# Kernel optimization log

Hardware: AMD Instinct MI355X
Metric: run time of the kernel (lower is better)

Reference implementation:

```python
import jax, jax.numpy as jnp
import numpy as np

D, H, HD, L, P, DF = 256, 8, 32, 4, 4, 1024
BS, NQ = 8, 900
SHAPES = np.array([[128, 128], [64, 64], [32, 32], [16, 16]], dtype=np.int64)
NV = int((SHAPES[:, 0] * SHAPES[:, 1]).sum())  # 21760


def setup_inputs():
    ks = jax.random.split(jax.random.key(0), 16)
    p = lambda i, s: jax.random.normal(ks[i], s, jnp.float32) * 0.02
    lsi = np.concatenate([[0], np.cumsum(SHAPES[:, 0] * SHAPES[:, 1])[:-1]]).astype(np.int64)
    return dict(
        tgt=jax.random.normal(ks[0], (BS, NQ, D), jnp.float32),
        query_pos=jax.random.normal(ks[1], (BS, NQ, D), jnp.float32),
        reference_points=jax.random.uniform(ks[2], (BS, NQ, L, 2), jnp.float32),
        src=jax.random.normal(ks[3], (BS, NV, D), jnp.float32),
        sa_in_w=p(4, (3 * D, D)), sa_in_b=jnp.zeros((3 * D,), jnp.float32),
        sa_out_w=p(5, (D, D)), sa_out_b=jnp.zeros((D,), jnp.float32),
        ln2_g=jnp.ones((D,), jnp.float32), ln2_b=jnp.zeros((D,), jnp.float32),
        off_w=p(6, (H * L * P * 2, D)),
        off_b=jax.random.uniform(ks[7], (H * L * P * 2,), jnp.float32, -2.0, 2.0),
        aw_w=p(8, (H * L * P, D)), aw_b=jnp.zeros((H * L * P,), jnp.float32),
        val_w=p(9, (D, D)), val_b=jnp.zeros((D,), jnp.float32),
        out_w=p(10, (D, D)), out_b=jnp.zeros((D,), jnp.float32),
        ln1_g=jnp.ones((D,), jnp.float32), ln1_b=jnp.zeros((D,), jnp.float32),
        ffn1_w=p(11, (DF, D)), ffn1_b=jnp.zeros((DF,), jnp.float32),
        ffn2_w=p(12, (D, DF)), ffn2_b=jnp.zeros((D,), jnp.float32),
        ln3_g=jnp.ones((D,), jnp.float32), ln3_b=jnp.zeros((D,), jnp.float32),
        spatial_shapes=SHAPES,
        level_start_index=lsi,
    )


def _ln(x, g, b):
    m = x.mean(-1, keepdims=True)
    v = ((x - m) ** 2).mean(-1, keepdims=True)
    return (x - m) * jax.lax.rsqrt(v + 1e-5) * g + b


def _msda_core(query, value, ref, off_w, off_b, aw_w, aw_b, spatial_shapes):
    # query: (bs,nq,D); value: (bs,NV,H,HD); ref: (bs,nq,L,2) normalized in [0,1]
    bs, nq, _ = query.shape
    off = (query @ off_w.T + off_b).reshape(bs, nq, H, L, P, 2)
    aw = jax.nn.softmax((query @ aw_w.T + aw_b).reshape(bs, nq, H, L * P), axis=-1)
    aw = aw.reshape(bs, nq, H, L, P)
    # offset normalizer is (W, H) per level
    norm = jnp.asarray(np.ascontiguousarray(spatial_shapes[:, ::-1]), jnp.float32)
    loc = ref[:, :, None, :, None, :] + off / norm[None, None, None, :, None, :]
    starts = np.concatenate([[0], np.cumsum(spatial_shapes[:, 0] * spatial_shapes[:, 1])])
    out = jnp.zeros((bs, nq, H, HD), query.dtype)
    for l in range(L):
        hh, ww = int(spatial_shapes[l, 0]), int(spatial_shapes[l, 1])
        v = value[:, int(starts[l]):int(starts[l + 1])].transpose(0, 2, 1, 3)  # (bs,H,hw,HD)
        lx = loc[:, :, :, l, :, 0] * ww - 0.5  # (bs,nq,H,P), align_corners=False
        ly = loc[:, :, :, l, :, 1] * hh - 0.5
        x0, y0 = jnp.floor(lx), jnp.floor(ly)
        tx, ty = lx - x0, ly - y0
        samp = jnp.zeros((bs, H, nq, P, HD), query.dtype)
        for dy, wy in ((0, 1.0 - ty), (1, ty)):
            for dx, wx in ((0, 1.0 - tx), (1, tx)):
                xi, yi = x0 + dx, y0 + dy
                valid = (xi >= 0) & (xi < ww) & (yi >= 0) & (yi < hh)  # zero padding
                idx = (jnp.clip(yi, 0, hh - 1) * ww + jnp.clip(xi, 0, ww - 1)).astype(jnp.int32)
                idxg = idx.transpose(0, 2, 1, 3).reshape(bs, H, nq * P, 1)  # (bs,H,nq*P,1)
                g = jnp.take_along_axis(v, idxg, axis=2).reshape(bs, H, nq, P, HD)
                w = (wy * wx * valid.astype(query.dtype)).transpose(0, 2, 1, 3)[..., None]
                samp = samp + g * w
        out = out + jnp.einsum('bhqpd,bqhp->bqhd', samp, aw[:, :, :, l, :])
    return out.reshape(bs, nq, H * HD)


def _forward(tgt, query_pos, reference_points, src,
             sa_in_w, sa_in_b, sa_out_w, sa_out_b, ln2_g, ln2_b,
             off_w, off_b, aw_w, aw_b, val_w, val_b, out_w, out_b, ln1_g, ln1_b,
             ffn1_w, ffn1_b, ffn2_w, ffn2_b, ln3_g, ln3_b,
             spatial_shapes):
    bs, nq, _ = tgt.shape
    # --- self attention (q=k=tgt+pos, v=tgt) ---
    qk = tgt + query_pos
    wq, wk, wv = sa_in_w[:D], sa_in_w[D:2 * D], sa_in_w[2 * D:]
    bq, bk, bv = sa_in_b[:D], sa_in_b[D:2 * D], sa_in_b[2 * D:]
    q = (qk @ wq.T + bq).reshape(bs, nq, H, HD)
    k = (qk @ wk.T + bk).reshape(bs, nq, H, HD)
    v = (tgt @ wv.T + bv).reshape(bs, nq, H, HD)
    attn = jax.nn.softmax(jnp.einsum('bqhd,bkhd->bhqk', q, k) / np.sqrt(HD).astype(np.float32), axis=-1)
    sa = jnp.einsum('bhqk,bkhd->bqhd', attn, v).reshape(bs, nq, D) @ sa_out_w.T + sa_out_b
    tgt = _ln(tgt + sa, ln2_g, ln2_b)
    # --- multi-scale deformable cross attention (mmcv: residual inside) ---
    value = (src @ val_w.T + val_b).reshape(bs, -1, H, HD)
    ca = _msda_core(tgt + query_pos, value, reference_points, off_w, off_b, aw_w, aw_b, spatial_shapes)
    ca = ca @ out_w.T + out_b + tgt  # mmcv MSDA adds identity internally
    tgt = _ln(tgt + ca, ln1_g, ln1_b)
    # --- FFN ---
    ffn = jax.nn.relu(tgt @ ffn1_w.T + ffn1_b) @ ffn2_w.T + ffn2_b
    return _ln(tgt + ffn, ln3_g, ln3_b)


def reference(tgt, query_pos, reference_points, src,
              sa_in_w, sa_in_b, sa_out_w, sa_out_b, ln2_g, ln2_b,
              off_w, off_b, aw_w, aw_b, val_w, val_b, out_w, out_b, ln1_g, ln1_b,
              ffn1_w, ffn1_b, ffn2_w, ffn2_b, ln3_g, ln3_b,
              spatial_shapes, level_start_index):
    del level_start_index  # level splits recomputed statically from spatial_shapes
    return _forward(tgt, query_pos, reference_points, src,
                    sa_in_w, sa_in_b, sa_out_w, sa_out_b, ln2_g, ln2_b,
                    off_w, off_b, aw_w, aw_b, val_w, val_b, out_w, out_b, ln1_g, ln1_b,
                    ffn1_w, ffn1_b, ffn2_w, ffn2_b, ln3_g, ln3_b,
                    spatial_shapes)
```

## Files before the change

kernel.cpp:

```cpp
#include <hip/hip_runtime.h>
#include <math.h>

#define D_   256
#define H_   8
#define HD_  32
#define L_   4
#define P_   4
#define DF_  1024
#define BS_  8
#define NQ_  900
#define NV_  21760
#define M1   (BS_*NQ_)
#define MV   (BS_*NV_)
#define QKVW 768
#define OAW  384
#define KS_  8
#define KCH  113

typedef __attribute__((ext_vector_type(8))) short short8v;
typedef __attribute__((ext_vector_type(4))) float float4v;
typedef unsigned short ushort_t;
typedef unsigned int uint_t;

__device__ __forceinline__ ushort_t f2bf(float f) {
    uint_t u = __float_as_uint(f);
    u += 0x7FFFu + ((u >> 16) & 1u);
    return (ushort_t)(u >> 16);
}
__device__ __forceinline__ float bf2f(ushort_t h) {
    return __uint_as_float(((uint_t)h) << 16);
}

template<bool ADD2, bool RELU, bool ADDRES>
__global__ __launch_bounds__(256) void gemm_mfma(const float* __restrict__ A,
                                                 const float* __restrict__ A2,
                                                 const float* __restrict__ Wt,
                                                 const float* __restrict__ bias,
                                                 const float* __restrict__ res,
                                                 float* __restrict__ C,
                                                 int M, int K, int ldc, int coffs)
{
    __shared__ short Al[8 * 64 * 8];
    __shared__ short Wl[8 * 4 * 64 * 8];

    const int tid = threadIdx.x;
    const int bm = blockIdx.y * 128, bn = blockIdx.x * 64;

    const int l = tid & 63, w = tid >> 6;
    const int mbase = (w & 1) * 4, nbase = (w >> 1) * 2;
    float4v acc[4][2];
    #pragma unroll
    for (int m = 0; m < 4; m++)
        #pragma unroll
        for (int n = 0; n < 2; n++)
            acc[m][n] = (float4v){0.f, 0.f, 0.f, 0.f};

    const int arow  = tid >> 1;
    const int arow_c = min(bm + arow, M - 1);
    const int khalf = (tid & 1) * 16;
    const float* ap  = A + (size_t)arow_c * K + khalf;
    const float* ap2 = ADD2 ? (A2 + (size_t)arow_c * K + khalf) : nullptr;

    const int wrow = tid >> 2;
    const int kq   = (tid & 3) * 64;

    for (int ks = 0; ks < K; ks += 256) {
        __syncthreads();
        {
            const float* wp = Wt + (size_t)(bn + wrow) * K + ks + kq;
            #pragma unroll
            for (int grp = 0; grp < 8; grp++) {
                float4 f0 = *(const float4*)(wp + grp * 8);
                float4 f1 = *(const float4*)(wp + grp * 8 + 4);
                short8v v;
                v[0] = (short)f2bf(f0.x); v[1] = (short)f2bf(f0.y);
                v[2] = (short)f2bf(f0.z); v[3] = (short)f2bf(f0.w);
                v[4] = (short)f2bf(f1.x); v[5] = (short)f2bf(f1.y);
                v[6] = (short)f2bf(f1.z); v[7] = (short)f2bf(f1.w);
                int kg = (tid & 3) * 8 + grp;
                int kc = kg >> 2, kin = kg & 3;
                int off = (((kc * 4 + (wrow >> 4)) * 64) + kin * 16 + (wrow & 15)) * 8;
                *(short8v*)&Wl[off] = v;
            }
        }
        float4 r0, r1, r2, r3;
        {
            const float* p = ap + ks;
            r0 = *(const float4*)(p + 0);  r1 = *(const float4*)(p + 4);
            r2 = *(const float4*)(p + 8);  r3 = *(const float4*)(p + 12);
            if (ADD2) {
                const float* p2 = ap2 + ks;
                float4 s0 = *(const float4*)(p2 + 0), s1 = *(const float4*)(p2 + 4);
                float4 s2 = *(const float4*)(p2 + 8), s3 = *(const float4*)(p2 + 12);
                r0.x += s0.x; r0.y += s0.y; r0.z += s0.z; r0.w += s0.w;
                r1.x += s1.x; r1.y += s1.y; r1.z += s1.z; r1.w += s1.w;
                r2.x += s2.x; r2.y += s2.y; r2.z += s2.z; r2.w += s2.w;
                r3.x += s3.x; r3.y += s3.y; r3.z += s3.z; r3.w += s3.w;
            }
        }

        for (int kc = 0; kc < 8; kc++) {
            {
                short8v v0, v1;
                v0[0] = (short)f2bf(r0.x); v0[1] = (short)f2bf(r0.y);
                v0[2] = (short)f2bf(r0.z); v0[3] = (short)f2bf(r0.w);
                v0[4] = (short)f2bf(r1.x); v0[5] = (short)f2bf(r1.y);
                v0[6] = (short)f2bf(r1.z); v0[7] = (short)f2bf(r1.w);
                v1[0] = (short)f2bf(r2.x); v1[1] = (short)f2bf(r2.y);
                v1[2] = (short)f2bf(r2.z); v1[3] = (short)f2bf(r2.w);
                v1[4] = (short)f2bf(r3.x); v1[5] = (short)f2bf(r3.y);
                v1[6] = (short)f2bf(r3.z); v1[7] = (short)f2bf(r3.w);
                int kg = (tid & 1) * 2;
                int off0 = (((arow >> 4) * 64) + kg * 16 + (arow & 15)) * 8;
                int off1 = (((arow >> 4) * 64) + (kg + 1) * 16 + (arow & 15)) * 8;
                *(short8v*)&Al[off0] = v0;
                *(short8v*)&Al[off1] = v1;
            }
            if (kc < 7) {
                const float* p = ap + ks + (kc + 1) * 32;
                r0 = *(const float4*)(p + 0);  r1 = *(const float4*)(p + 4);
                r2 = *(const float4*)(p + 8);  r3 = *(const float4*)(p + 12);
                if (ADD2) {
                    const float* p2 = ap2 + ks + (kc + 1) * 32;
                    float4 s0 = *(const float4*)(p2 + 0), s1 = *(const float4*)(p2 + 4);
                    float4 s2 = *(const float4*)(p2 + 8), s3 = *(const float4*)(p2 + 12);
                    r0.x += s0.x; r0.y += s0.y; r0.z += s0.z; r0.w += s0.w;
                    r1.x += s1.x; r1.y += s1.y; r1.z += s1.z; r1.w += s1.w;
                    r2.x += s2.x; r2.y += s2.y; r2.z += s2.z; r2.w += s2.w;
                    r3.x += s3.x; r3.y += s3.y; r3.z += s3.z; r3.w += s3.w;
                }
            }
            __syncthreads();

            short8v af0 = *(const short8v*)&Al[((mbase + 0) * 64 + l) * 8];
            short8v af1 = *(const short8v*)&Al[((mbase + 1) * 64 + l) * 8];
            short8v af2 = *(const short8v*)&Al[((mbase + 2) * 64 + l) * 8];
            short8v af3 = *(const short8v*)&Al[((mbase + 3) * 64 + l) * 8];
            short8v bf0 = *(const short8v*)&Wl[((kc * 4 + nbase + 0) * 64 + l) * 8];
            short8v bf1 = *(const short8v*)&Wl[((kc * 4 + nbase + 1) * 64 + l) * 8];

            acc[0][0] = __builtin_amdgcn_mfma_f32_16x16x32_bf16(af0, bf0, acc[0][0], 0, 0, 0);
            acc[0][1] = __builtin_amdgcn_mfma_f32_16x16x32_bf16(af0, bf1, acc[0][1], 0, 0, 0);
            acc[1][0] = __builtin_amdgcn_mfma_f32_16x16x32_bf16(af1, bf0, acc[1][0], 0, 0, 0);
            acc[1][1] = __builtin_amdgcn_mfma_f32_16x16x32_bf16(af1, bf1, acc[1][1], 0, 0, 0);
            acc[2][0] = __builtin_amdgcn_mfma_f32_16x16x32_bf16(af2, bf0, acc[2][0], 0, 0, 0);
            acc[2][1] = __builtin_amdgcn_mfma_f32_16x16x32_bf16(af2, bf1, acc[2][1], 0, 0, 0);
            acc[3][0] = __builtin_amdgcn_mfma_f32_16x16x32_bf16(af3, bf0, acc[3][0], 0, 0, 0);
            acc[3][1] = __builtin_amdgcn_mfma_f32_16x16x32_bf16(af3, bf1, acc[3][1], 0, 0, 0);

            __syncthreads();
        }
    }

    #pragma unroll
    for (int n = 0; n < 2; n++) {
        int gc = bn + nbase * 16 + n * 16 + (l & 15);
        float bc = bias[gc];
        #pragma unroll
        for (int m = 0; m < 4; m++) {
            int gr0 = bm + mbase * 16 + m * 16 + (l >> 4) * 4;
            #pragma unroll
            for (int r = 0; r < 4; r++) {
                int gr = gr0 + r;
                if (gr >= M) continue;
                float v = acc[m][n][r] + bc;
                if (ADDRES) v += res[(size_t)gr * ldc + coffs + gc];
                if (RELU)   v = fmaxf(v, 0.f);
                C[(size_t)gr * ldc + coffs + gc] = v;
            }
        }
    }
}

__global__ __launch_bounds__(256) void gemm_val_bf16(const float* __restrict__ A,
                                                     const float* __restrict__ Wt,
                                                     const float* __restrict__ bias,
                                                     ushort_t* __restrict__ C)
{
    __shared__ short Al[8 * 64 * 8];
    __shared__ short Wl[8 * 4 * 64 * 8];

    const int tid = threadIdx.x;
    const int bm = blockIdx.y * 128, bn = blockIdx.x * 64;

    {
        const int wrow = tid >> 2;
        const int kq   = (tid & 3) * 64;
        const float* wp = Wt + (size_t)(bn + wrow) * D_ + kq;
        #pragma unroll
        for (int grp = 0; grp < 8; grp++) {
            float4 f0 = *(const float4*)(wp + grp * 8);
            float4 f1 = *(const float4*)(wp + grp * 8 + 4);
            short8v v;
            v[0] = (short)f2bf(f0.x); v[1] = (short)f2bf(f0.y);
            v[2] = (short)f2bf(f0.z); v[3] = (short)f2bf(f0.w);
            v[4] = (short)f2bf(f1.x); v[5] = (short)f2bf(f1.y);
            v[6] = (short)f2bf(f1.z); v[7] = (short)f2bf(f1.w);
            int kg = (tid & 3) * 8 + grp;
            int kc = kg >> 2, kin = kg & 3;
            int off = (((kc * 4 + (wrow >> 4)) * 64) + kin * 16 + (wrow & 15)) * 8;
            *(short8v*)&Wl[off] = v;
        }
    }

    const int arow = tid >> 1;
    const int khalf = (tid & 1) * 16;
    const float* ap = A + (size_t)(bm + arow) * D_ + khalf;

    float4 r0, r1, r2, r3;
    r0 = *(const float4*)(ap + 0);  r1 = *(const float4*)(ap + 4);
    r2 = *(const float4*)(ap + 8);  r3 = *(const float4*)(ap + 12);

    const int l = tid & 63, w = tid >> 6;
    const int mbase = (w & 1) * 4, nbase = (w >> 1) * 2;
    float4v acc[4][2];
    #pragma unroll
    for (int m = 0; m < 4; m++)
        #pragma unroll
        for (int n = 0; n < 2; n++)
            acc[m][n] = (float4v){0.f, 0.f, 0.f, 0.f};

    __syncthreads();

    for (int kc = 0; kc < 8; kc++) {
        {
            short8v v0, v1;
            v0[0] = (short)f2bf(r0.x); v0[1] = (short)f2bf(r0.y);
            v0[2] = (short)f2bf(r0.z); v0[3] = (short)f2bf(r0.w);
            v0[4] = (short)f2bf(r1.x); v0[5] = (short)f2bf(r1.y);
            v0[6] = (short)f2bf(r1.z); v0[7] = (short)f2bf(r1.w);
            v1[0] = (short)f2bf(r2.x); v1[1] = (short)f2bf(r2.y);
            v1[2] = (short)f2bf(r2.z); v1[3] = (short)f2bf(r2.w);
            v1[4] = (short)f2bf(r3.x); v1[5] = (short)f2bf(r3.y);
            v1[6] = (short)f2bf(r3.z); v1[7] = (short)f2bf(r3.w);
            int kg = (tid & 1) * 2;
            int off0 = (((arow >> 4) * 64) + kg * 16 + (arow & 15)) * 8;
            int off1 = (((arow >> 4) * 64) + (kg + 1) * 16 + (arow & 15)) * 8;
            *(short8v*)&Al[off0] = v0;
            *(short8v*)&Al[off1] = v1;
        }
        if (kc < 7) {
            const float* np = ap + (kc + 1) * 32;
            r0 = *(const float4*)(np + 0);  r1 = *(const float4*)(np + 4);
            r2 = *(const float4*)(np + 8);  r3 = *(const float4*)(np + 12);
        }
        __syncthreads();

        short8v af0 = *(const short8v*)&Al[((mbase + 0) * 64 + l) * 8];
        short8v af1 = *(const short8v*)&Al[((mbase + 1) * 64 + l) * 8];
        short8v af2 = *(const short8v*)&Al[((mbase + 2) * 64 + l) * 8];
        short8v af3 = *(const short8v*)&Al[((mbase + 3) * 64 + l) * 8];
        short8v bf0 = *(const short8v*)&Wl[((kc * 4 + nbase + 0) * 64 + l) * 8];
        short8v bf1 = *(const short8v*)&Wl[((kc * 4 + nbase + 1) * 64 + l) * 8];

        acc[0][0] = __builtin_amdgcn_mfma_f32_16x16x32_bf16(af0, bf0, acc[0][0], 0, 0, 0);
        acc[0][1] = __builtin_amdgcn_mfma_f32_16x16x32_bf16(af0, bf1, acc[0][1], 0, 0, 0);
        acc[1][0] = __builtin_amdgcn_mfma_f32_16x16x32_bf16(af1, bf0, acc[1][0], 0, 0, 0);
        acc[1][1] = __builtin_amdgcn_mfma_f32_16x16x32_bf16(af1, bf1, acc[1][1], 0, 0, 0);
        acc[2][0] = __builtin_amdgcn_mfma_f32_16x16x32_bf16(af2, bf0, acc[2][0], 0, 0, 0);
        acc[2][1] = __builtin_amdgcn_mfma_f32_16x16x32_bf16(af2, bf1, acc[2][1], 0, 0, 0);
        acc[3][0] = __builtin_amdgcn_mfma_f32_16x16x32_bf16(af3, bf0, acc[3][0], 0, 0, 0);
        acc[3][1] = __builtin_amdgcn_mfma_f32_16x16x32_bf16(af3, bf1, acc[3][1], 0, 0, 0);

        __syncthreads();
    }

    #pragma unroll
    for (int n = 0; n < 2; n++) {
        int gc = bn + nbase * 16 + n * 16 + (l & 15);
        float bc = bias[gc];
        #pragma unroll
        for (int m = 0; m < 4; m++) {
            int gr = bm + mbase * 16 + m * 16 + (l >> 4) * 4;
            #pragma unroll
            for (int r = 0; r < 4; r++)
                C[(size_t)(gr + r) * D_ + gc] = f2bf(acc[m][n][r] + bc);
        }
    }
}

#define ATK 64
__global__ __launch_bounds__(128) void attn_kernel(const float* __restrict__ QKV,
                                                   float* __restrict__ pml,
                                                   float* __restrict__ pacc)
{
    const int b = blockIdx.z, h = blockIdx.y;
    const int qb = blockIdx.x & 7, ks = blockIdx.x >> 3;
    const int q0 = qb * 128;
    const int kstart = ks * KCH;
    const int kend   = min(NQ_, kstart + KCH);
    const int tid  = threadIdx.x;
    const int wave = tid >> 6, lane = tid & 63;
    const int qi = lane & 31, half = lane >> 5;

    __shared__ float Ksm[ATK][HD_];
    __shared__ float Vsm[ATK][HD_];

    const int q_a = q0 + wave * 64 + qi * 2;
    const int q_b = q_a + 1;
    const int qa_c = min(q_a, NQ_ - 1);
    const int qb_c = min(q_b, NQ_ - 1);

    const float scale = 0.17677669529663687f;
    float Qa[16], Qb[16];
    {
        const float* pa = QKV + ((size_t)(b * NQ_ + qa_c)) * QKVW + h * HD_ + half * 16;
        const float* pb = QKV + ((size_t)(b * NQ_ + qb_c)) * QKVW + h * HD_ + half * 16;
        #pragma unroll
        for (int i = 0; i < 16; i += 4) {
            float4 va = *(const float4*)&pa[i];
            float4 vb = *(const float4*)&pb[i];
            Qa[i] = va.x * scale; Qa[i+1] = va.y * scale; Qa[i+2] = va.z * scale; Qa[i+3] = va.w * scale;
            Qb[i] = vb.x * scale; Qb[i+1] = vb.y * scale; Qb[i+2] = vb.z * scale; Qb[i+3] = vb.w * scale;
        }
    }

    float ma = -INFINITY, la = 0.f, mb = -INFINITY, lb = 0.f;
    float aa[16], ab[16];
    #pragma unroll
    for (int i = 0; i < 16; i++) { aa[i] = 0.f; ab[i] = 0.f; }

    for (int j0 = kstart; j0 < kend; j0 += ATK) {
        const int jn = min(ATK, kend - j0);
        __syncthreads();
        for (int f = tid; f < ATK * HD_ / 4; f += 128) {
            int j = f >> 3, d4 = (f & 7) << 2;
            if (j < jn) {
                const float* kp = QKV + ((size_t)(b * NQ_ + j0 + j)) * QKVW + 256 + h * HD_ + d4;
                *(float4*)&Ksm[j][d4] = *(const float4*)kp;
                *(float4*)&Vsm[j][d4] = *(const float4*)(kp + 256);
            }
        }
        __syncthreads();

        for (int j = 0; j < jn; j++) {
            float kr[16];
            #pragma unroll
            for (int i = 0; i < 16; i += 4) {
                float4 kv = *(const float4*)&Ksm[j][half * 16 + i];
                kr[i] = kv.x; kr[i+1] = kv.y; kr[i+2] = kv.z; kr[i+3] = kv.w;
            }
            float sa0 = 0.f, sa1 = 0.f, sa2 = 0.f, sa3 = 0.f;
            float sb0 = 0.f, sb1 = 0.f, sb2 = 0.f, sb3 = 0.f;
            #pragma unroll
            for (int i = 0; i < 16; i += 4) {
                sa0 += Qa[i] * kr[i];     sa1 += Qa[i+1] * kr[i+1];
                sa2 += Qa[i+2] * kr[i+2]; sa3 += Qa[i+3] * kr[i+3];
                sb0 += Qb[i] * kr[i];     sb1 += Qb[i+1] * kr[i+1];
                sb2 += Qb[i+2] * kr[i+2]; sb3 += Qb[i+3] * kr[i+3];
            }
            float sA = (sa0 + sa1) + (sa2 + sa3);
            float sB = (sb0 + sb1) + (sb2 + sb3);
            sA += __shfl_xor(sA, 32);
            sB += __shfl_xor(sB, 32);

            float vr[16];
            #pragma unroll
            for (int i = 0; i < 16; i += 4) {
                float4 vv = *(const float4*)&Vsm[j][half * 16 + i];
                vr[i] = vv.x; vr[i+1] = vv.y; vr[i+2] = vv.z; vr[i+3] = vv.w;
            }

            if (sA > ma) {
                float sc = __expf(ma - sA);
                la *= sc;
                #pragma unroll
                for (int i = 0; i < 16; i++) aa[i] *= sc;
                ma = sA;
            }
            float pA = __expf(sA - ma);
            la += pA;
            #pragma unroll
            for (int i = 0; i < 16; i++) aa[i] += pA * vr[i];

            if (sB > mb) {
                float sc = __expf(mb - sB);
                lb *= sc;
                #pragma unroll
                for (int i = 0; i < 16; i++) ab[i] *= sc;
                mb = sB;
            }
            float pB = __expf(sB - mb);
            lb += pB;
            #pragma unroll
            for (int i = 0; i < 16; i++) ab[i] += pB * vr[i];
        }
    }

    const int bh = b * H_ + h;
    if (q_a < NQ_) {
        size_t base = (((size_t)bh * KS_ + ks) * NQ_ + q_a) * 32 + half * 16;
        #pragma unroll
        for (int i = 0; i < 16; i += 4) {
            float4 v = make_float4(aa[i], aa[i+1], aa[i+2], aa[i+3]);
            *(float4*)&pacc[base + i] = v;
        }
        if (half == 0) {
            size_t mb_ = (((size_t)bh * KS_ + ks) * NQ_ + q_a) * 2;
            pml[mb_] = ma; pml[mb_ + 1] = la;
        }
    }
    if (q_b < NQ_) {
        size_t base = (((size_t)bh * KS_ + ks) * NQ_ + q_b) * 32 + half * 16;
        #pragma unroll
        for (int i = 0; i < 16; i += 4) {
            float4 v = make_float4(ab[i], ab[i+1], ab[i+2], ab[i+3]);
            *(float4*)&pacc[base + i] = v;
        }
        if (half == 0) {
            size_t mb_ = (((size_t)bh * KS_ + ks) * NQ_ + q_b) * 2;
            pml[mb_] = mb; pml[mb_ + 1] = lb;
        }
    }
}

__global__ __launch_bounds__(256) void attn_combine(const float* __restrict__ pml,
                                                    const float* __restrict__ pacc,
                                                    float* __restrict__ SA)
{
    const int g  = threadIdx.x >> 5;
    const int ch = threadIdx.x & 31;
    const int t  = blockIdx.x * 8 + g;
    const int bh = t / NQ_, q = t - bh * NQ_;

    float mv[KS_], lv[KS_];
    float M = -INFINITY;
    #pragma unroll
    for (int i = 0; i < KS_; i++) {
        size_t mb = (((size_t)bh * KS_ + i) * NQ_ + q) * 2;
        mv[i] = pml[mb]; lv[i] = pml[mb + 1];
        M = fmaxf(M, mv[i]);
    }
    float L = 0.f, acc = 0.f;
    #pragma unroll
    for (int i = 0; i < KS_; i++) {
        float wgt = __expf(mv[i] - M);
        L += lv[i] * wgt;
        acc += wgt * pacc[(((size_t)bh * KS_ + i) * NQ_ + q) * 32 + ch];
    }
    const int b = bh >> 3, h = bh & 7;
    SA[((size_t)(b * NQ_ + q)) * D_ + h * HD_ + ch] = acc / L;
}

__global__ __launch_bounds__(64) void ln_kernel(const float* __restrict__ X,
                                                const float* __restrict__ Y,
                                                const float* __restrict__ g,
                                                const float* __restrict__ bt,
                                                float* __restrict__ out)
{
    const int row = blockIdx.x;
    const int lane = threadIdx.x;
    const size_t base = (size_t)row * D_ + lane * 4;
    float4 x = *(const float4*)&X[base];
    float4 y = *(const float4*)&Y[base];
    float v0 = x.x + y.x, v1 = x.y + y.y, v2 = x.z + y.z, v3 = x.w + y.w;
    float s = v0 + v1 + v2 + v3;
    #pragma unroll
    for (int o = 32; o; o >>= 1) s += __shfl_xor(s, o);
    float mean = s * (1.f / D_);
    float d0 = v0 - mean, d1 = v1 - mean, d2 = v2 - mean, d3 = v3 - mean;
    float ss = d0 * d0 + d1 * d1 + d2 * d2 + d3 * d3;
    #pragma unroll
    for (int o = 32; o; o >>= 1) ss += __shfl_xor(ss, o);
    float rstd = rsqrtf(ss * (1.f / D_) + 1e-5f);
    float4 gg = *(const float4*)&g[lane * 4];
    float4 bb = *(const float4*)&bt[lane * 4];
    float4 o4 = make_float4(d0 * rstd * gg.x + bb.x, d1 * rstd * gg.y + bb.y,
                            d2 * rstd * gg.z + bb.z, d3 * rstd * gg.w + bb.w);
    *(float4*)&out[base] = o4;
}

__global__ __launch_bounds__(256) void aw_softmax_kernel(float* __restrict__ offaw)
{
    int t = blockIdx.x * 256 + threadIdx.x;
    if (t >= M1 * H_) return;
    const int bq = t >> 3, h = t & 7;
    float* p = offaw + (size_t)bq * OAW + 256 + h * 16;
    float v[16];
    #pragma unroll
    for (int i = 0; i < 16; i += 4) {
        float4 q = *(const float4*)&p[i];
        v[i] = q.x; v[i+1] = q.y; v[i+2] = q.z; v[i+3] = q.w;
    }
    float m = v[0];
    #pragma unroll
    for (int i = 1; i < 16; i++) m = fmaxf(m, v[i]);
    float s = 0.f;
    #pragma unroll
    for (int i = 0; i < 16; i++) { v[i] = __expf(v[i] - m); s += v[i]; }
    float inv = 1.f / s;
    #pragma unroll
    for (int i = 0; i < 16; i += 4) {
        float4 q = make_float4(v[i] * inv, v[i+1] * inv, v[i+2] * inv, v[i+3] * inv);
        *(float4*)&p[i] = q;
    }
}

__global__ __launch_bounds__(256) void msda_kernel(const ushort_t* __restrict__ value,
                                                   const float* __restrict__ offaw,
                                                   const float* __restrict__ ref,
                                                   float* __restrict__ out)
{
    const int g    = threadIdx.x >> 5;
    const int lane = threadIdx.x & 31;
    const int t    = blockIdx.x * 8 + g;
    const int h  = t & 7;
    const int bq = t >> 3;
    const int b  = bq / NQ_;
    const float* offp = offaw + (size_t)bq * OAW + h * (L_ * P_ * 2);
    const float* awp  = offaw + (size_t)bq * OAW + 256 + h * (L_ * P_);
    const float* refp = ref + (size_t)bq * (L_ * 2);
    const ushort_t* vb = value + ((size_t)b * NV_) * D_ + h * HD_ + lane;

    float acc = 0.f;
    const int LW[4] = {128, 64, 32, 16};
    const int LS[4] = {0, 16384, 20480, 21504};

    #pragma unroll
    for (int l = 0; l < L_; l++) {
        const int wi = LW[l];
        const float Wf = (float)wi;
        float rx = refp[2 * l], ry = refp[2 * l + 1];
        #pragma unroll
        for (int p = 0; p < P_; p++) {
            float ox = offp[(l * P_ + p) * 2];
            float oy = offp[(l * P_ + p) * 2 + 1];
            float a  = awp[l * P_ + p];
            float lx = rx * Wf + ox - 0.5f;
            float ly = ry * Wf + oy - 0.5f;
            float x0f = floorf(lx), y0f = floorf(ly);
            float fx = lx - x0f, fy = ly - y0f;
            int x0 = (int)x0f, y0 = (int)y0f;
            #pragma unroll
            for (int dy = 0; dy < 2; dy++) {
                int yi = y0 + dy;
                if (yi < 0 || yi >= wi) continue;
                float wy = dy ? fy : 1.f - fy;
                #pragma unroll
                for (int dx = 0; dx < 2; dx++) {
                    int xi = x0 + dx;
                    if (xi < 0 || xi >= wi) continue;
                    float w = wy * (dx ? fx : 1.f - fx) * a;
                    acc += w * bf2f(vb[(size_t)(LS[l] + yi * wi + xi) * D_]);
                }
            }
        }
    }
    out[(size_t)bq * D_ + h * HD_ + lane] = acc;
}

extern "C" void kernel_launch(void* const* d_in, const int* in_sizes, int n_in,
                              void* d_out, int out_size, void* d_ws, size_t ws_size,
                              hipStream_t stream)
{
    const float* tgt      = (const float*)d_in[0];
    const float* qpos     = (const float*)d_in[1];
    const float* ref      = (const float*)d_in[2];
    const float* src      = (const float*)d_in[3];
    const float* sa_in_w  = (const float*)d_in[4];
    const float* sa_in_b  = (const float*)d_in[5];
    const float* sa_out_w = (const float*)d_in[6];
    const float* sa_out_b = (const float*)d_in[7];
    const float* ln2_g    = (const float*)d_in[8];
    const float* ln2_b    = (const float*)d_in[9];
    const float* off_w    = (const float*)d_in[10];
    const float* off_b    = (const float*)d_in[11];
    const float* aw_w     = (const float*)d_in[12];
    const float* aw_b     = (const float*)d_in[13];
    const float* val_w    = (const float*)d_in[14];
    const float* val_b    = (const float*)d_in[15];
    const float* out_w    = (const float*)d_in[16];
    const float* out_b    = (const float*)d_in[17];
    const float* ln1_g    = (const float*)d_in[18];
    const float* ln1_b    = (const float*)d_in[19];
    const float* ffn1_w   = (const float*)d_in[20];
    const float* ffn1_b   = (const float*)d_in[21];
    const float* ffn2_w   = (const float*)d_in[22];
    const float* ffn2_b   = (const float*)d_in[23];
    const float* ln3_g    = (const float*)d_in[24];
    const float* ln3_b    = (const float*)d_in[25];

    float* ws      = (float*)d_ws;
    ushort_t* value = (ushort_t*)ws;
    float* qkv   = ws + 22282240;
    float* battn = qkv + (size_t)M1 * QKVW;
    float* b2    = battn + (size_t)M1 * D_;
    float* b4    = b2 + (size_t)M1 * D_;
    float* pml   = b4 + (size_t)M1 * D_;
    float* pacc  = pml + (size_t)M1 * H_ * KS_ * 2;
    float* bsa   = qkv;
    float* offaw = qkv + (size_t)M1 * D_;
    float* bmsda = qkv;
    float* bca   = battn;
    float* hid   = pml;
    float* bffn  = qkv;
    float* out   = (float*)d_out;

    const dim3 g57_4(4, 57), g57_8(8, 57), g57_2(2, 57), g57_16(16, 57);

    gemm_mfma<true,  false, false><<<g57_8, 256, 0, stream>>>(
        tgt, qpos, sa_in_w, sa_in_b, nullptr, qkv, M1, D_, QKVW, 0);
    gemm_mfma<false, false, false><<<g57_4, 256, 0, stream>>>(
        tgt, nullptr, sa_in_w + 2 * D_ * D_, sa_in_b + 2 * D_, nullptr, qkv, M1, D_, QKVW, 512);
    gemm_val_bf16<<<dim3(D_ / 64, MV / 128), 256, 0, stream>>>(
        src, val_w, val_b, value);
    attn_kernel<<<dim3(8 * KS_, H_, BS_), 128, 0, stream>>>(qkv, pml, pacc);
    attn_combine<<<M1 * H_ / 8, 256, 0, stream>>>(pml, pacc, battn);
    gemm_mfma<false, false, false><<<g57_4, 256, 0, stream>>>(
        battn, nullptr, sa_out_w, sa_out_b, nullptr, bsa, M1, D_, D_, 0);
    ln_kernel<<<M1, 64, 0, stream>>>(tgt, bsa, ln2_g, ln2_b, b2);
    gemm_mfma<true, false, false><<<g57_4, 256, 0, stream>>>(
        b2, qpos, off_w, off_b, nullptr, offaw, M1, D_, OAW, 0);
    gemm_mfma<true, false, false><<<g57_2, 256, 0, stream>>>(
        b2, qpos, aw_w, aw_b, nullptr, offaw, M1, D_, OAW, 256);
    aw_softmax_kernel<<<(M1 * H_ + 255) / 256, 256, 0, stream>>>(offaw);
    msda_kernel<<<M1 * H_ / 8, 256, 0, stream>>>(value, offaw, ref, bmsda);
    gemm_mfma<false, false, true><<<g57_4, 256, 0, stream>>>(
        bmsda, nullptr, out_w, out_b, b2, bca, M1, D_, D_, 0);
    ln_kernel<<<M1, 64, 0, stream>>>(b2, bca, ln1_g, ln1_b, b4);
    gemm_mfma<false, true,  false><<<g57_16, 256, 0, stream>>>(
        b4, nullptr, ffn1_w, ffn1_b, nullptr, hid, M1, D_, DF_, 0);
    gemm_mfma<false, false, false><<<g57_4, 256, 0, stream>>>(
        hid, nullptr, ffn2_w, ffn2_b, nullptr, bffn, M1, DF_, D_, 0);
    ln_kernel<<<M1, 64, 0, stream>>>(b4, bffn, ln3_g, ln3_b, out);
}
```

Before: 868.9 us.

## Replace split-K scalar self-attention with single-pass bf16 MFMA flash attention

Replaces the scalar FP32 self-attention kernel, which split keys into 8 chunks and then needed a separate combine kernel, with one flash-attention kernel. It computes QK^T and PV using bf16 16x16x32 MFMA instructions with an online softmax over 64-key tiles. This removes the partial-result buffers and the combine launch and moves the dot products onto matrix cores. In exchange Q, K, V and P are rounded to bf16, which lowers precision. Grid parallelism also drops to 15x64 blocks, each walking all keys sequentially.

```diff
diff --git a/kernel.cpp b/kernel.cpp
--- a/kernel.cpp
+++ b/kernel.cpp
@@ -14,8 +14,7 @@
 #define MV   (BS_*NV_)
 #define QKVW 768
 #define OAW  384
-#define KS_  8
-#define KCH  113
+#define KT_  64
 
 typedef __attribute__((ext_vector_type(8))) short short8v;
 typedef __attribute__((ext_vector_type(4))) float float4v;
@@ -279,167 +278,146 @@
     }
 }
 
-#define ATK 64
-__global__ __launch_bounds__(128) void attn_kernel(const float* __restrict__ QKV,
-                                                   float* __restrict__ pml,
-                                                   float* __restrict__ pacc)
+__global__ __launch_bounds__(256) void attn_mfma(const float* __restrict__ QKV,
+                                                 float* __restrict__ SA)
 {
-    const int b = blockIdx.z, h = blockIdx.y;
-    const int qb = blockIdx.x & 7, ks = blockIdx.x >> 3;
-    const int q0 = qb * 128;
-    const int kstart = ks * KCH;
-    const int kend   = min(NQ_, kstart + KCH);
-    const int tid  = threadIdx.x;
-    const int wave = tid >> 6, lane = tid & 63;
-    const int qi = lane & 31, half = lane >> 5;
-
-    __shared__ float Ksm[ATK][HD_];
-    __shared__ float Vsm[ATK][HD_];
-
-    const int q_a = q0 + wave * 64 + qi * 2;
-    const int q_b = q_a + 1;
-    const int qa_c = min(q_a, NQ_ - 1);
-    const int qb_c = min(q_b, NQ_ - 1);
+    const int bh = blockIdx.y;
+    const int b = bh >> 3, h = bh & 7;
+    const int q0 = blockIdx.x * 64;
+    const int tid = threadIdx.x, l = tid & 63, w = tid >> 6;
+
+    __shared__ short Ql[4][64][8];
+    __shared__ short Kl[4][64][8];
+    __shared__ short Vl[2][2][64][8];
+    __shared__ short Pl[4][2][64][8];
+    __shared__ float cs[4][16];
 
     const float scale = 0.17677669529663687f;
-    float Qa[16], Qb[16];
+
     {
-        const float* pa = QKV + ((size_t)(b * NQ_ + qa_c)) * QKVW + h * HD_ + half * 16;
-        const float* pb = QKV + ((size_t)(b * NQ_ + qb_c)) * QKVW + h * HD_ + half * 16;
-        #pragma unroll
-        for (int i = 0; i < 16; i += 4) {
-            float4 va = *(const float4*)&pa[i];
-            float4 vb = *(const float4*)&pb[i];
-            Qa[i] = va.x * scale; Qa[i+1] = va.y * scale; Qa[i+2] = va.z * scale; Qa[i+3] = va.w * scale;
-            Qb[i] = vb.x * scale; Qb[i+1] = vb.y * scale; Qb[i+2] = vb.z * scale; Qb[i+3] = vb.w * scale;
-        }
-    }
-
-    float ma = -INFINITY, la = 0.f, mb = -INFINITY, lb = 0.f;
-    float aa[16], ab[16];
-    #pragma unroll
-    for (int i = 0; i < 16; i++) { aa[i] = 0.f; ab[i] = 0.f; }
-
-    for (int j0 = kstart; j0 < kend; j0 += ATK) {
-        const int jn = min(ATK, kend - j0);
+        const int qrow = tid >> 2, dgrp = tid & 3;
+        const int qg = min(q0 + qrow, NQ_ - 1);
+        const float* qp = QKV + ((size_t)(b * NQ_ + qg)) * QKVW + h * HD_ + dgrp * 8;
+        float4 f0 = *(const float4*)qp, f1 = *(const float4*)(qp + 4);
+        short8v v;
+        v[0] = (short)f2bf(f0.x * scale); v[1] = (short)f2bf(f0.y * scale);
+        v[2] = (short)f2bf(f0.z * scale); v[3] = (short)f2bf(f0.w * scale);
+        v[4] = (short)f2bf(f1.x * scale); v[5] = (short)f2bf(f1.y * scale);
+        v[6] = (short)f2bf(f1.z * scale); v[7] = (short)f2bf(f1.w * scale);
+        *(short8v*)&Ql[qrow >> 4][(qrow & 15) + 16 * dgrp][0] = v;
+    }
+    __syncthreads();
+    const short8v qf = *(const short8v*)&Ql[w][l][0];
+
+    float m = -INFINITY, lsum = 0.f;
+    float4v o0 = (float4v){0.f, 0.f, 0.f, 0.f};
+    float4v o1 = (float4v){0.f, 0.f, 0.f, 0.f};
+
+    for (int kt0 = 0; kt0 < NQ_; kt0 += KT_) {
+        {
+            const int krow = tid >> 2, dgrp = tid & 3;
+            const int key = kt0 + krow;
+            float4 f0 = make_float4(0.f,0.f,0.f,0.f), f1 = f0;
+            float4 g0 = f0, g1 = f0;
+            if (key < NQ_) {
+                const float* kp = QKV + ((size_t)(b * NQ_ + key)) * QKVW + 256 + h * HD_ + dgrp * 8;
+                f0 = *(const float4*)kp;       f1 = *(const float4*)(kp + 4);
+                g0 = *(const float4*)(kp+256); g1 = *(const float4*)(kp + 260);
+            }
+            short8v v;
+            v[0] = (short)f2bf(f0.x); v[1] = (short)f2bf(f0.y);
+            v[2] = (short)f2bf(f0.z); v[3] = (short)f2bf(f0.w);
+            v[4] = (short)f2bf(f1.x); v[5] = (short)f2bf(f1.y);
+            v[6] = (short)f2bf(f1.z); v[7] = (short)f2bf(f1.w);
+            *(short8v*)&Kl[krow >> 4][(krow & 15) + 16 * dgrp][0] = v;
+
+            const int kf = krow >> 5;
+            const int lb = 16 * ((krow & 31) >> 3);
+            const int j  = krow & 7;
+            const int d0 = dgrp * 8;
+            Vl[kf][(d0+0)>>4][((d0+0)&15)+lb][j] = (short)f2bf(g0.x);
+            Vl[kf][(d0+1)>>4][((d0+1)&15)+lb][j] = (short)f2bf(g0.y);
+            Vl[kf][(d0+2)>>4][((d0+2)&15)+lb][j] = (short)f2bf(g0.z);
+            Vl[kf][(d0+3)>>4][((d0+3)&15)+lb][j] = (short)f2bf(g0.w);
+            Vl[kf][(d0+4)>>4][((d0+4)&15)+lb][j] = (short)f2bf(g1.x);
+            Vl[kf][(d0+5)>>4][((d0+5)&15)+lb][j] = (short)f2bf(g1.y);
+            Vl[kf][(d0+6)>>4][((d0+6)&15)+lb][j] = (short)f2bf(g1.z);
+            Vl[kf][(d0+7)>>4][((d0+7)&15)+lb][j] = (short)f2bf(g1.w);
+        }
         __syncthreads();
-        for (int f = tid; f < ATK * HD_ / 4; f += 128) {
-            int j = f >> 3, d4 = (f & 7) << 2;
-            if (j < jn) {
-                const float* kp = QKV + ((size_t)(b * NQ_ + j0 + j)) * QKVW + 256 + h * HD_ + d4;
-                *(float4*)&Ksm[j][d4] = *(const float4*)kp;
-                *(float4*)&Vsm[j][d4] = *(const float4*)(kp + 256);
-            }
+
+        float4v s[4];
+        #pragma unroll
+        for (int f = 0; f < 4; f++) {
+            short8v kfr = *(const short8v*)&Kl[f][l][0];
+            s[f] = __builtin_amdgcn_mfma_f32_16x16x32_bf16(
+                kfr, qf, (float4v){0.f, 0.f, 0.f, 0.f}, 0, 0, 0);
+        }
+        if (kt0 + KT_ > NQ_) {
+            #pragma unroll
+            for (int f = 0; f < 4; f++)
+                #pragma unroll
+                for (int r = 0; r < 4; r++)
+                    if (kt0 + f * 16 + (l >> 4) * 4 + r >= NQ_) s[f][r] = -1e30f;
+        }
+
+        float tm = -1e30f;
+        #pragma unroll
+        for (int f = 0; f < 4; f++)
+            #pragma unroll
+            for (int r = 0; r < 4; r++) tm = fmaxf(tm, s[f][r]);
+        tm = fmaxf(tm, __shfl_xor(tm, 16));
+        tm = fmaxf(tm, __shfl_xor(tm, 32));
+        float mnew = fmaxf(m, tm);
+        float c = __expf(m - mnew);
+        m = mnew;
+        float ps = 0.f;
+        #pragma unroll
+        for (int f = 0; f < 4; f++)
+            #pragma unroll
+            for (int r = 0; r < 4; r++) {
+                float p = __expf(s[f][r] - m);
+                s[f][r] = p; ps += p;
+            }
+        ps += __shfl_xor(ps, 16);
+        ps += __shfl_xor(ps, 32);
+        lsum = lsum * c + ps;
+        if ((l >> 4) == 0) cs[w][l & 15] = c;
+        float4 c4 = *(const float4*)&cs[w][(l >> 4) * 4];
+        o0[0] *= c4.x; o0[1] *= c4.y; o0[2] *= c4.z; o0[3] *= c4.w;
+        o1[0] *= c4.x; o1[1] *= c4.y; o1[2] *= c4.z; o1[3] *= c4.w;
+
+        #pragma unroll
+        for (int f = 0; f < 4; f++) {
+            uint_t lo = (uint_t)f2bf(s[f][0]) | ((uint_t)f2bf(s[f][1]) << 16);
+            uint_t hi = (uint_t)f2bf(s[f][2]) | ((uint_t)f2bf(s[f][3]) << 16);
+            int lp = (l & 15) + 16 * ((f & 1) * 2 + ((l >> 4) >> 1));
+            int j0 = ((l >> 4) & 1) * 4;
+            *(uint2*)&Pl[w][f >> 1][lp][j0] = make_uint2(lo, hi);
+        }
+        #pragma unroll
+        for (int kf = 0; kf < 2; kf++) {
+            short8v pa = *(const short8v*)&Pl[w][kf][l][0];
+            short8v v0 = *(const short8v*)&Vl[kf][0][l][0];
+            short8v v1 = *(const short8v*)&Vl[kf][1][l][0];
+            o0 = __builtin_amdgcn_mfma_f32_16x16x32_bf16(pa, v0, o0, 0, 0, 0);
+            o1 = __builtin_amdgcn_mfma_f32_16x16x32_bf16(pa, v1, o1, 0, 0, 0);
         }
         __syncthreads();
-
-        for (int j = 0; j < jn; j++) {
-            float kr[16];
-            #pragma unroll
-            for (int i = 0; i < 16; i += 4) {
-                float4 kv = *(const float4*)&Ksm[j][half * 16 + i];
-                kr[i] = kv.x; kr[i+1] = kv.y; kr[i+2] = kv.z; kr[i+3] = kv.w;
-            }
-            float sa0 = 0.f, sa1 = 0.f, sa2 = 0.f, sa3 = 0.f;
-            float sb0 = 0.f, sb1 = 0.f, sb2 = 0.f, sb3 = 0.f;
-            #pragma unroll
-            for (int i = 0; i < 16; i += 4) {
-                sa0 += Qa[i] * kr[i];     sa1 += Qa[i+1] * kr[i+1];
-                sa2 += Qa[i+2] * kr[i+2]; sa3 += Qa[i+3] * kr[i+3];
-                sb0 += Qb[i] * kr[i];     sb1 += Qb[i+1] * kr[i+1];
-                sb2 += Qb[i+2] * kr[i+2]; sb3 += Qb[i+3] * kr[i+3];
-            }
-            float sA = (sa0 + sa1) + (sa2 + sa3);
-            float sB = (sb0 + sb1) + (sb2 + sb3);
-            sA += __shfl_xor(sA, 32);
-            sB += __shfl_xor(sB, 32);
-
-            float vr[16];
-            #pragma unroll
-            for (int i = 0; i < 16; i += 4) {
-                float4 vv = *(const float4*)&Vsm[j][half * 16 + i];
-                vr[i] = vv.x; vr[i+1] = vv.y; vr[i+2] = vv.z; vr[i+3] = vv.w;
-            }
-
-            if (sA > ma) {
-                float sc = __expf(ma - sA);
-                la *= sc;
-                #pragma unroll
-                for (int i = 0; i < 16; i++) aa[i] *= sc;
-                ma = sA;
-            }
-            float pA = __expf(sA - ma);
-            la += pA;
-            #pragma unroll
-            for (int i = 0; i < 16; i++) aa[i] += pA * vr[i];
-
-            if (sB > mb) {
-                float sc = __expf(mb - sB);
-                lb *= sc;
-                #pragma unroll
-                for (int i = 0; i < 16; i++) ab[i] *= sc;
-                mb = sB;
-            }
-            float pB = __expf(sB - mb);
-            lb += pB;
-            #pragma unroll
-            for (int i = 0; i < 16; i++) ab[i] += pB * vr[i];
-        }
-    }
-
-    const int bh = b * H_ + h;
-    if (q_a < NQ_) {
-        size_t base = (((size_t)bh * KS_ + ks) * NQ_ + q_a) * 32 + half * 16;
-        #pragma unroll
-        for (int i = 0; i < 16; i += 4) {
-            float4 v = make_float4(aa[i], aa[i+1], aa[i+2], aa[i+3]);
-            *(float4*)&pacc[base + i] = v;
-        }
-        if (half == 0) {
-            size_t mb_ = (((size_t)bh * KS_ + ks) * NQ_ + q_a) * 2;
-            pml[mb_] = ma; pml[mb_ + 1] = la;
-        }
-    }
-    if (q_b < NQ_) {
-        size_t base = (((size_t)bh * KS_ + ks) * NQ_ + q_b) * 32 + half * 16;
-        #pragma unroll
-        for (int i = 0; i < 16; i += 4) {
-            float4 v = make_float4(ab[i], ab[i+1], ab[i+2], ab[i+3]);
-            *(float4*)&pacc[base + i] = v;
-        }
-        if (half == 0) {
-            size_t mb_ = (((size_t)bh * KS_ + ks) * NQ_ + q_b) * 2;
-            pml[mb_] = mb; pml[mb_ + 1] = lb;
-        }
-    }
-}
-
-__global__ __launch_bounds__(256) void attn_combine(const float* __restrict__ pml,
-                                                    const float* __restrict__ pacc,
-                                                    float* __restrict__ SA)
-{
-    const int g  = threadIdx.x >> 5;
-    const int ch = threadIdx.x & 31;
-    const int t  = blockIdx.x * 8 + g;
-    const int bh = t / NQ_, q = t - bh * NQ_;
-
-    float mv[KS_], lv[KS_];
-    float M = -INFINITY;
-    #pragma unroll
-    for (int i = 0; i < KS_; i++) {
-        size_t mb = (((size_t)bh * KS_ + i) * NQ_ + q) * 2;
-        mv[i] = pml[mb]; lv[i] = pml[mb + 1];
-        M = fmaxf(M, mv[i]);
-    }
-    float L = 0.f, acc = 0.f;
-    #pragma unroll
-    for (int i = 0; i < KS_; i++) {
-        float wgt = __expf(mv[i] - M);
-        L += lv[i] * wgt;
-        acc += wgt * pacc[(((size_t)bh * KS_ + i) * NQ_ + q) * 32 + ch];
-    }
-    const int b = bh >> 3, h = bh & 7;
-    SA[((size_t)(b * NQ_ + q)) * D_ + h * HD_ + ch] = acc / L;
+    }
+
+    if ((l >> 4) == 0) cs[w][l & 15] = lsum;
+    float4 l4 = *(const float4*)&cs[w][(l >> 4) * 4];
+    float linv[4] = {1.f / l4.x, 1.f / l4.y, 1.f / l4.z, 1.f / l4.w};
+    #pragma unroll
+    for (int r = 0; r < 4; r++) {
+        int qg = q0 + w * 16 + (l >> 4) * 4 + r;
+        if (qg < NQ_) {
+            float* op = SA + ((size_t)(b * NQ_ + qg)) * D_ + h * HD_ + (l & 15);
+            op[0]  = o0[r] * linv[r];
+            op[16] = o1[r] * linv[r];
+        }
+    }
 }
 
 __global__ __launch_bounds__(64) void ln_kernel(const float* __restrict__ X,
@@ -586,13 +564,11 @@
     float* battn = qkv + (size_t)M1 * QKVW;
     float* b2    = battn + (size_t)M1 * D_;
     float* b4    = b2 + (size_t)M1 * D_;
-    float* pml   = b4 + (size_t)M1 * D_;
-    float* pacc  = pml + (size_t)M1 * H_ * KS_ * 2;
+    float* hid   = b4 + (size_t)M1 * D_;
     float* bsa   = qkv;
     float* offaw = qkv + (size_t)M1 * D_;
     float* bmsda = qkv;
     float* bca   = battn;
-    float* hid   = pml;
     float* bffn  = qkv;
     float* out   = (float*)d_out;
 
@@ -604,8 +580,7 @@
         tgt, nullptr, sa_in_w + 2 * D_ * D_, sa_in_b + 2 * D_, nullptr, qkv, M1, D_, QKVW, 512);
     gemm_val_bf16<<<dim3(D_ / 64, MV / 128), 256, 0, stream>>>(
         src, val_w, val_b, value);
-    attn_kernel<<<dim3(8 * KS_, H_, BS_), 128, 0, stream>>>(qkv, pml, pacc);
-    attn_combine<<<M1 * H_ / 8, 256, 0, stream>>>(pml, pacc, battn);
+    attn_mfma<<<dim3((NQ_ + 63) / 64, BS_ * H_), 256, 0, stream>>>(qkv, battn);
     gemm_mfma<false, false, false><<<g57_4, 256, 0, stream>>>(
         battn, nullptr, sa_out_w, sa_out_b, nullptr, bsa, M1, D_, D_, 0);
     ln_kernel<<<M1, 64, 0, stream>>>(tgt, bsa, ln2_g, ln2_b, b2);
```

Measured after the change: 722.9 us. 16.8% less time.
